# Performance work log

Measured on AMD Instinct MI355X. Metric: run time of the kernel, lower is better.

Reference implementation:

```python
import jax, jax.numpy as jnp
import numpy as np

P = 30000      # nodes (WSI patches)
DIN = 1536     # input feature dim
DOUT = 256     # output dim
HEADS = 2
C = DOUT // HEADS  # per-head channels = 128
E = 320000     # edges (before self-loops)
NEG_SLOPE = 0.2


def setup_inputs() -> dict:
    key = jax.random.key(0)
    ks = jax.random.split(key, 12)
    g = lambda k, shape: jax.random.normal(k, shape, jnp.float32) * 0.02
    return {
        "x": jax.random.normal(ks[0], (P, DIN), jnp.float32),
        "edge_index": jax.random.randint(ks[1], (2, E), 0, P),
        "W1l": g(ks[2], (DIN, DOUT)), "b1l": jnp.zeros((DOUT,), jnp.float32),
        "W1r": g(ks[3], (DIN, DOUT)), "b1r": jnp.zeros((DOUT,), jnp.float32),
        "att1": g(ks[4], (HEADS, C)), "bias1": jnp.zeros((DOUT,), jnp.float32),
        "W2l": g(ks[5], (DOUT, DOUT)), "b2l": jnp.zeros((DOUT,), jnp.float32),
        "W2r": g(ks[6], (DOUT, DOUT)), "b2r": jnp.zeros((DOUT,), jnp.float32),
        "att2": g(ks[7], (HEADS, C)), "bias2": jnp.zeros((DOUT,), jnp.float32),
        "ln1_g": jnp.ones((DOUT,), jnp.float32), "ln1_b": jnp.zeros((DOUT,), jnp.float32),
        "ln2_g": jnp.ones((DOUT,), jnp.float32), "ln2_b": jnp.zeros((DOUT,), jnp.float32),
        "resW": g(ks[8], (DIN, DOUT)), "resb": jnp.zeros((DOUT,), jnp.float32),
    }


def layer_norm(h, g, b, eps=1e-5):
    mu = h.mean(-1, keepdims=True)
    var = ((h - mu) ** 2).mean(-1, keepdims=True)
    return (h - mu) * jax.lax.rsqrt(var + eps) * g + b


def gatv2(x, src, dst, Wl, bl, Wr, br, att, bias):
    # PyG GATv2Conv: lin_l on source j, lin_r on target i,
    # e_ij = att . LeakyReLU(xl[j] + xr[i]); softmax over incoming edges of i;
    # out_i = sum_j alpha_ij * xl[j]  (heads concatenated) + bias.
    n = x.shape[0]
    xl = (x @ Wl + bl).reshape(n, HEADS, C)
    xr = (x @ Wr + br).reshape(n, HEADS, C)
    m = jax.nn.leaky_relu(xl[src] + xr[dst], NEG_SLOPE)      # (Etot, H, C)
    e = jnp.einsum('ehc,hc->eh', m, att)                     # (Etot, H)
    emax = jax.ops.segment_max(e, dst, num_segments=n)       # stable segment softmax
    ex = jnp.exp(e - emax[dst])
    den = jax.ops.segment_sum(ex, dst, num_segments=n)
    alpha = ex / den[dst]                                    # (Etot, H)
    out = jax.ops.segment_sum(xl[src] * alpha[..., None], dst, num_segments=n)
    return out.reshape(n, HEADS * C) + bias


def reference(x, edge_index, W1l, b1l, W1r, b1r, att1, bias1,
              W2l, b2l, W2r, b2r, att2, bias2,
              ln1_g, ln1_b, ln2_g, ln2_b, resW, resb):
    loops = jnp.arange(P)
    src = jnp.concatenate([edge_index[0], loops])  # add self loops
    dst = jnp.concatenate([edge_index[1], loops])

    h1 = gatv2(x, src, dst, W1l, b1l, W1r, b1r, att1, bias1)
    h1 = jax.nn.elu(layer_norm(h1, ln1_g, ln1_b)) + (x @ resW + resb)

    h2 = gatv2(h1, src, dst, W2l, b2l, W2r, b2r, att2, bias2)
    h2 = jax.nn.elu(layer_norm(h2, ln2_g, ln2_b)) + h2 * 0 + h1 + (h2 - h1) * 0 if False else jax.nn.elu(layer_norm(h2, ln2_g, ln2_b)) + h1
    # JK-max combine of the two layer outputs
    return jnp.maximum(h1, h2)
```

## Files before the change

### kernel.cpp

```cpp
#include <hip/hip_runtime.h>
#include <math.h>

#define P_NODES 30000
#define P_PAD   30080
#define DIN_    1536
#define DOUT_   256
#define E_EDGES 320000
#define ET      (E_EDGES + P_NODES)
#define NEG     0.2f
#define BIG_NEG (-1e30f)

typedef float  f32x4  __attribute__((ext_vector_type(4)));
typedef __bf16 bf16x8 __attribute__((ext_vector_type(8)));
typedef __bf16 bf16x4 __attribute__((ext_vector_type(4)));

__device__ __forceinline__ int swz_col(int c, int row) {
    return (c & ~63) | ((((c >> 3) ^ row) & 7) << 3) | (c & 7);
}

__device__ __forceinline__ int xcd_swz(int orig, int nwg) {
    int q = nwg >> 3, r = nwg & 7;
    int xcd = orig & 7, idx = orig >> 3;
    return (xcd < r ? xcd * (q + 1) : r * (q + 1) + (xcd - r) * q) + idx;
}

__global__ __launch_bounds__(256)
void cast_x(const float* __restrict__ x, __bf16* __restrict__ XB)
{
    int idx = blockIdx.x * 256 + threadIdx.x;
    if (idx >= P_PAD * 192) return;
    int row = idx / 192;
    int c = (idx - row * 192) * 8;
    int cs = swz_col(c, row);
    bf16x8 o;
    if (row < P_NODES) {
        f32x4 v0 = *(const f32x4*)(x + (size_t)row * DIN_ + c);
        f32x4 v1 = *(const f32x4*)(x + (size_t)row * DIN_ + c + 4);
        #pragma unroll
        for (int j = 0; j < 4; ++j) { o[j] = (__bf16)v0[j]; o[j + 4] = (__bf16)v1[j]; }
    } else {
        #pragma unroll
        for (int j = 0; j < 8; ++j) o[j] = (__bf16)0.f;
    }
    *(bf16x8*)(XB + (size_t)row * DIN_ + cs) = o;
}

__global__ __launch_bounds__(256)
void prep_w1(const float* __restrict__ W1l, const float* __restrict__ W1r,
             const float* __restrict__ resW, __bf16* __restrict__ WT1)
{
    int idx = blockIdx.x * 256 + threadIdx.x;
    if (idx >= DIN_ * 192) return;
    int k = idx / 192;
    int n0 = (idx - k * 192) * 4;
    const float* src; int col;
    if (n0 < 256)      { src = W1l;  col = n0; }
    else if (n0 < 512) { src = W1r;  col = n0 - 256; }
    else               { src = resW; col = n0 - 512; }
    f32x4 v = *(const f32x4*)(src + (size_t)k * DOUT_ + col);
    #pragma unroll
    for (int j = 0; j < 4; ++j) {
        int n = n0 + j;
        WT1[(size_t)n * DIN_ + swz_col(k, n)] = (__bf16)v[j];
    }
}

__global__ __launch_bounds__(256)
void prep_w2(const float* __restrict__ W2l, const float* __restrict__ W2r,
             __bf16* __restrict__ WT2)
{
    int idx = blockIdx.x * 256 + threadIdx.x;
    if (idx >= 256 * 128) return;
    int k = idx / 128;
    int n0 = (idx - k * 128) * 4;
    const float* src; int col;
    if (n0 < 256) { src = W2l; col = n0; }
    else          { src = W2r; col = n0 - 256; }
    f32x4 v = *(const f32x4*)(src + (size_t)k * DOUT_ + col);
    #pragma unroll
    for (int j = 0; j < 4; ++j) {
        int n = n0 + j;
        WT2[(size_t)n * DOUT_ + swz_col(k, n)] = (__bf16)v[j];
    }
}

__global__ void prep_bias(const float* b1l, const float* b1r, const float* resb,
                          const float* b2l, const float* b2r,
                          float* B1, float* B2)
{
    int t = threadIdx.x;
    if (t < 256)      B1[t] = b1l[t];
    else if (t < 512) B1[t] = b1r[t - 256];
    else if (t < 768) B1[t] = resb[t - 512];
    if (t < 256)      B2[t] = b2l[t];
    else if (t < 512) B2[t] = b2r[t - 256];
}

__global__ void init_deg(int* deg)
{
    int i = blockIdx.x * 256 + threadIdx.x;
    if (i < P_NODES) deg[i] = 1;
}

__global__ void hist_kernel(const int* __restrict__ dst, int* __restrict__ deg)
{
    int e = blockIdx.x * 256 + threadIdx.x;
    if (e < E_EDGES) atomicAdd(&deg[dst[e]], 1);
}

__global__ __launch_bounds__(1024)
void scan_kernel(const int* __restrict__ deg, int* __restrict__ offs, int* __restrict__ pos)
{
    __shared__ int sb[1024];
    const int t = threadIdx.x;
    const int base = t * 30;
    int ldv[30];
    int lsum = 0;
    #pragma unroll
    for (int i = 0; i < 30; ++i) {
        int idx = base + i;
        int v = (idx < P_NODES) ? deg[idx] : 0;
        ldv[i] = v; lsum += v;
    }
    sb[t] = lsum; __syncthreads();
    for (int off = 1; off < 1024; off <<= 1) {
        int v = (t >= off) ? sb[t - off] : 0;
        __syncthreads();
        sb[t] += v;
        __syncthreads();
    }
    int excl = sb[t] - lsum;
    #pragma unroll
    for (int i = 0; i < 30; ++i) {
        int idx = base + i;
        if (idx < P_NODES) { offs[idx] = excl; pos[idx] = excl; excl += ldv[i]; }
    }
    if (t == 0) offs[P_NODES] = ET;
}

__global__ void scatter_kernel(const int* __restrict__ ei, int* __restrict__ pos,
                               int* __restrict__ srcs)
{
    int tgt = blockIdx.x * 256 + threadIdx.x;
    if (tgt < E_EDGES) {
        int s = ei[tgt];
        int d = ei[E_EDGES + tgt];
        int p = atomicAdd(&pos[d], 1);
        srcs[p] = s;
    } else if (tgt < ET) {
        int i = tgt - E_EDGES;
        int p = atomicAdd(&pos[i], 1);
        srcs[p] = i;
    }
}

template<int EPI>
__global__ __launch_bounds__(256)
void gemm_kernel(const __bf16* __restrict__ A, const __bf16* __restrict__ WT,
                 const float* __restrict__ bias,
                 __bf16* __restrict__ Cb, float* __restrict__ Cf,
                 int M, int N, int K, int ntiles)
{
    __shared__ __align__(16) __bf16 As[128 * 64];
    __shared__ __align__(16) __bf16 Bs[128 * 64];

    const int bid = xcd_swz(blockIdx.x, gridDim.x);
    const int mt = bid / ntiles, nt = bid - mt * ntiles;
    const int grow = mt * 128, gcol = nt * 128;
    const int t = threadIdx.x;
    const int lane = t & 63, wave = t >> 6;
    const int wr = wave >> 1, wc = wave & 1;
    const int fr = lane & 15, kg = lane >> 4;
    const int frs = fr & 7;

    const __bf16* agp = A  + (size_t)(grow + (t >> 3)) * K + (t & 7) * 8;
    const __bf16* bgp = WT + (size_t)(gcol + (t >> 3)) * K + (t & 7) * 8;
    const size_t rstep = (size_t)32 * K;
    char* lA = (char*)As + wave * 1024;
    char* lB = (char*)Bs + wave * 1024;

    f32x4 acc[4][4] = {};

    for (int k0 = 0; k0 < K; k0 += 64) {
        __syncthreads();
        #pragma unroll
        for (int i = 0; i < 4; ++i) {
            __builtin_amdgcn_global_load_lds(
                (const __attribute__((address_space(1))) void*)(agp + i * rstep + k0),
                (__attribute__((address_space(3))) void*)(lA + i * 4096), 16, 0, 0);
            __builtin_amdgcn_global_load_lds(
                (const __attribute__((address_space(1))) void*)(bgp + i * rstep + k0),
                (__attribute__((address_space(3))) void*)(lB + i * 4096), 16, 0, 0);
        }
        __syncthreads();

        #pragma unroll
        for (int ks = 0; ks < 2; ++ks) {
            bf16x8 af[4], bv[4];
            #pragma unroll
            for (int mi = 0; mi < 4; ++mi)
                af[mi] = *(const bf16x8*)&As[(wr * 64 + mi * 16 + fr) * 64 + (((ks * 4 + kg) ^ frs)) * 8];
            #pragma unroll
            for (int ni = 0; ni < 4; ++ni)
                bv[ni] = *(const bf16x8*)&Bs[(wc * 64 + ni * 16 + fr) * 64 + (((ks * 4 + kg) ^ frs)) * 8];
            #pragma unroll
            for (int mi = 0; mi < 4; ++mi)
                #pragma unroll
                for (int ni = 0; ni < 4; ++ni)
                    acc[mi][ni] = __builtin_amdgcn_mfma_f32_16x16x32_bf16(af[mi], bv[ni], acc[mi][ni], 0, 0, 0);
        }
    }

    #pragma unroll
    for (int mi = 0; mi < 4; ++mi) {
        #pragma unroll
        for (int ni = 0; ni < 4; ++ni) {
            int col = gcol + wc * 64 + ni * 16 + fr;
            float bvv = bias[col];
            #pragma unroll
            for (int j = 0; j < 4; ++j) {
                int row = grow + wr * 64 + mi * 16 + kg * 4 + j;
                if (row < M) {
                    float v = acc[mi][ni][j] + bvv;
                    if (EPI == 0) {
                        if (col < 512) Cb[(size_t)row * 512 + col] = (__bf16)v;
                        else           Cf[(size_t)row * 256 + col - 512] = v;
                    } else {
                        Cb[(size_t)row * 512 + col] = (__bf16)v;
                    }
                }
            }
        }
    }
}

template<int LAYER>
__global__ __launch_bounds__(256)
void gat_fused(const __bf16* __restrict__ XLXR,
               const int* __restrict__ offs, const int* __restrict__ srcs,
               const float* __restrict__ att, const float* __restrict__ bias,
               const float* __restrict__ lng, const float* __restrict__ lnb,
               const float* __restrict__ AUX,
               float* __restrict__ OutF, __bf16* __restrict__ OutB)
{
    const int node = blockIdx.x * 4 + (threadIdx.x >> 6);
    const int lane = threadIdx.x & 63;
    const int grp = lane >> 4, l = lane & 15;
    const int ch0 = l * 8, ch1 = 128 + l * 8;

    bf16x8 xr0b = *(const bf16x8*)(XLXR + (size_t)node * 512 + 256 + ch0);
    bf16x8 xr1b = *(const bf16x8*)(XLXR + (size_t)node * 512 + 256 + ch1);
    float xr0[8], xr1[8], at0[8], at1[8];
    #pragma unroll
    for (int j = 0; j < 8; ++j) { xr0[j] = (float)xr0b[j]; xr1[j] = (float)xr1b[j]; }
    *(f32x4*)(at0)     = *(const f32x4*)(att + ch0);
    *(f32x4*)(at0 + 4) = *(const f32x4*)(att + ch0 + 4);
    *(f32x4*)(at1)     = *(const f32x4*)(att + ch1);
    *(f32x4*)(at1 + 4) = *(const f32x4*)(att + ch1 + 4);

    float m0 = BIG_NEG, m1 = BIG_NEG, den0 = 0.f, den1 = 0.f;
    float acc0[8] = {}, acc1[8] = {};

    const int e0 = offs[node], e1 = offs[node + 1];
    for (int eb = e0; eb < e1; eb += 4) {
        int e = eb + grp;
        bool valid = e < e1;
        int ee = valid ? e : e1 - 1;
        int s = srcs[ee];
        const __bf16* xp = XLXR + (size_t)s * 512;
        bf16x8 a0 = *(const bf16x8*)(xp + ch0);
        bf16x8 a1 = *(const bf16x8*)(xp + ch1);
        float xl0[8], xl1[8];
        float p0 = 0.f, p1 = 0.f;
        #pragma unroll
        for (int j = 0; j < 8; ++j) {
            xl0[j] = (float)a0[j];
            float tt = xl0[j] + xr0[j];
            float lr = tt > 0.f ? tt : NEG * tt;
            p0 = fmaf(at0[j], lr, p0);
            xl1[j] = (float)a1[j];
            float t1 = xl1[j] + xr1[j];
            float l1 = t1 > 0.f ? t1 : NEG * t1;
            p1 = fmaf(at1[j], l1, p1);
        }
        #pragma unroll
        for (int w = 1; w < 16; w <<= 1) {
            p0 += __shfl_xor(p0, w);
            p1 += __shfl_xor(p1, w);
        }
        if (!valid) { p0 = BIG_NEG; p1 = BIG_NEG; }
        float nm0 = fmaxf(m0, p0), nm1 = fmaxf(m1, p1);
        float sc0 = __expf(m0 - nm0), wv0 = __expf(p0 - nm0);
        float sc1 = __expf(m1 - nm1), wv1 = __expf(p1 - nm1);
        den0 = den0 * sc0 + wv0;
        den1 = den1 * sc1 + wv1;
        #pragma unroll
        for (int j = 0; j < 8; ++j) {
            acc0[j] = acc0[j] * sc0 + wv0 * xl0[j];
            acc1[j] = acc1[j] * sc1 + wv1 * xl1[j];
        }
        m0 = nm0; m1 = nm1;
    }

    #pragma unroll
    for (int w = 16; w <= 32; w <<= 1) {
        float mb0 = __shfl_xor(m0, w), db0 = __shfl_xor(den0, w);
        float mb1 = __shfl_xor(m1, w), db1 = __shfl_xor(den1, w);
        float M0 = fmaxf(m0, mb0), M1 = fmaxf(m1, mb1);
        float sa0 = __expf(m0 - M0), sb0 = __expf(mb0 - M0);
        float sa1 = __expf(m1 - M1), sb1 = __expf(mb1 - M1);
        den0 = den0 * sa0 + db0 * sb0;
        den1 = den1 * sa1 + db1 * sb1;
        #pragma unroll
        for (int j = 0; j < 8; ++j) {
            float ab0 = __shfl_xor(acc0[j], w);
            float ab1 = __shfl_xor(acc1[j], w);
            acc0[j] = acc0[j] * sa0 + ab0 * sb0;
            acc1[j] = acc1[j] * sa1 + ab1 * sb1;
        }
        m0 = M0; m1 = M1;
    }

    float inv0 = 1.f / den0, inv1 = 1.f / den1;
    float o0[8], o1[8];
    #pragma unroll
    for (int j = 0; j < 8; ++j) {
        o0[j] = acc0[j] * inv0 + bias[ch0 + j];
        o1[j] = acc1[j] * inv1 + bias[ch1 + j];
    }

    float s = 0.f;
    #pragma unroll
    for (int j = 0; j < 8; ++j) s += o0[j] + o1[j];
    #pragma unroll
    for (int w = 1; w < 16; w <<= 1) s += __shfl_xor(s, w);
    float mu = s * (1.f / 256.f);
    float sq = 0.f;
    #pragma unroll
    for (int j = 0; j < 8; ++j) {
        o0[j] -= mu; o1[j] -= mu;
        sq += o0[j] * o0[j] + o1[j] * o1[j];
    }
    #pragma unroll
    for (int w = 1; w < 16; w <<= 1) sq += __shfl_xor(sq, w);
    float rs = rsqrtf(sq * (1.f / 256.f) + 1e-5f);

    float g0[8], g1[8], bb0[8], bb1[8], x0[8], x1[8];
    *(f32x4*)(g0)      = *(const f32x4*)(lng + ch0);
    *(f32x4*)(g0 + 4)  = *(const f32x4*)(lng + ch0 + 4);
    *(f32x4*)(g1)      = *(const f32x4*)(lng + ch1);
    *(f32x4*)(g1 + 4)  = *(const f32x4*)(lng + ch1 + 4);
    *(f32x4*)(bb0)     = *(const f32x4*)(lnb + ch0);
    *(f32x4*)(bb0 + 4) = *(const f32x4*)(lnb + ch0 + 4);
    *(f32x4*)(bb1)     = *(const f32x4*)(lnb + ch1);
    *(f32x4*)(bb1 + 4) = *(const f32x4*)(lnb + ch1 + 4);
    *(f32x4*)(x0)      = *(const f32x4*)(AUX + (size_t)node * 256 + ch0);
    *(f32x4*)(x0 + 4)  = *(const f32x4*)(AUX + (size_t)node * 256 + ch0 + 4);
    *(f32x4*)(x1)      = *(const f32x4*)(AUX + (size_t)node * 256 + ch1);
    *(f32x4*)(x1 + 4)  = *(const f32x4*)(AUX + (size_t)node * 256 + ch1 + 4);

    float r0[8], r1[8];
    #pragma unroll
    for (int j = 0; j < 8; ++j) {
        float y0 = o0[j] * rs * g0[j] + bb0[j];
        float y1 = o1[j] * rs * g1[j] + bb1[j];
        float e0v = y0 > 0.f ? y0 : __expf(y0) - 1.f;
        float e1v = y1 > 0.f ? y1 : __expf(y1) - 1.f;
        if (LAYER == 1) {
            r0[j] = e0v + x0[j];
            r1[j] = e1v + x1[j];
        } else {
            float h20 = e0v + x0[j];
            float h21 = e1v + x1[j];
            r0[j] = fmaxf(x0[j], h20);
            r1[j] = fmaxf(x1[j], h21);
        }
    }

    if (grp == 0) {
        float* op = OutF + (size_t)node * 256;
        *(f32x4*)(op + ch0)     = *(f32x4*)(r0);
        *(f32x4*)(op + ch0 + 4) = *(f32x4*)(r0 + 4);
        *(f32x4*)(op + ch1)     = *(f32x4*)(r1);
        *(f32x4*)(op + ch1 + 4) = *(f32x4*)(r1 + 4);
        if (LAYER == 1) {
            bf16x8 hb0, hb1;
            #pragma unroll
            for (int j = 0; j < 8; ++j) { hb0[j] = (__bf16)r0[j]; hb1[j] = (__bf16)r1[j]; }
            *(bf16x8*)(OutB + (size_t)node * 256 + swz_col(ch0, node)) = hb0;
            *(bf16x8*)(OutB + (size_t)node * 256 + swz_col(ch1, node)) = hb1;
        }
    }
}

__global__ void pad_h1b(__bf16* __restrict__ H1B)
{
    int i = blockIdx.x * 256 + threadIdx.x;
    if (i >= (P_PAD - P_NODES) * 32) return;
    int row = P_NODES + (i >> 5);
    int c = (i & 31) * 8;
    bf16x8 z;
    #pragma unroll
    for (int j = 0; j < 8; ++j) z[j] = (__bf16)0.f;
    *(bf16x8*)(H1B + (size_t)row * 256 + c) = z;
}

extern "C" void kernel_launch(void* const* d_in, const int* in_sizes, int n_in,
                              void* d_out, int out_size, void* d_ws, size_t ws_size,
                              hipStream_t stream)
{
    const float* x     = (const float*)d_in[0];
    const int*   ei    = (const int*)d_in[1];
    const float* W1l   = (const float*)d_in[2];
    const float* b1l   = (const float*)d_in[3];
    const float* W1r   = (const float*)d_in[4];
    const float* b1r   = (const float*)d_in[5];
    const float* att1  = (const float*)d_in[6];
    const float* bias1 = (const float*)d_in[7];
    const float* W2l   = (const float*)d_in[8];
    const float* b2l   = (const float*)d_in[9];
    const float* W2r   = (const float*)d_in[10];
    const float* b2r   = (const float*)d_in[11];
    const float* att2  = (const float*)d_in[12];
    const float* bias2 = (const float*)d_in[13];
    const float* ln1g  = (const float*)d_in[14];
    const float* ln1b  = (const float*)d_in[15];
    const float* ln2g  = (const float*)d_in[16];
    const float* ln2b  = (const float*)d_in[17];
    const float* resW  = (const float*)d_in[18];
    const float* resb  = (const float*)d_in[19];
    float* out = (float*)d_out;

    char* w = (char*)d_ws;
    auto alloc = [&](size_t bytes) {
        char* r = w;
        w += (bytes + 255) & ~(size_t)255;
        return r;
    };
    __bf16* XB    = (__bf16*)alloc((size_t)P_PAD * DIN_ * 2);
    __bf16* XLR1  = (__bf16*)alloc((size_t)P_NODES * 512 * 2);
    float*  RES   = (float*)alloc((size_t)P_NODES * 256 * 4);
    float*  H1    = (float*)alloc((size_t)P_NODES * 256 * 4);
    __bf16* WT1   = (__bf16*)alloc((size_t)768 * DIN_ * 2);
    __bf16* WT2   = (__bf16*)alloc((size_t)512 * DOUT_ * 2);
    float*  BIAS1 = (float*)alloc(768 * 4);
    float*  BIAS2 = (float*)alloc(512 * 4);
    int*    deg   = (int*)alloc((size_t)P_NODES * 4);
    int*    offs  = (int*)alloc((size_t)(P_NODES + 1) * 4);
    int*    pos   = (int*)alloc((size_t)(P_NODES + 1) * 4);
    int*    srcs  = (int*)alloc((size_t)ET * 4);

    __bf16* XLR2 = (__bf16*)XB;
    __bf16* H1B  = (__bf16*)((char*)XB + (size_t)32 * 1024 * 1024);

    cast_x<<<(P_PAD * 192 + 255) / 256, 256, 0, stream>>>(x, XB);
    prep_w1<<<(DIN_ * 192 + 255) / 256, 256, 0, stream>>>(W1l, W1r, resW, WT1);
    prep_w2<<<(256 * 128 + 255) / 256, 256, 0, stream>>>(W2l, W2r, WT2);
    prep_bias<<<1, 1024, 0, stream>>>(b1l, b1r, resb, b2l, b2r, BIAS1, BIAS2);
    init_deg<<<(P_NODES + 255) / 256, 256, 0, stream>>>(deg);
    hist_kernel<<<(E_EDGES + 255) / 256, 256, 0, stream>>>(ei + E_EDGES, deg);
    scan_kernel<<<1, 1024, 0, stream>>>(deg, offs, pos);
    scatter_kernel<<<(ET + 255) / 256, 256, 0, stream>>>(ei, pos, srcs);

    const int mtiles = P_PAD / 128;

    gemm_kernel<0><<<mtiles * 6, 256, 0, stream>>>(XB, WT1, BIAS1, XLR1, RES, P_NODES, 768, DIN_, 6);
    gat_fused<1><<<P_NODES / 4, 256, 0, stream>>>(XLR1, offs, srcs, att1, bias1,
                                                  ln1g, ln1b, RES, H1, H1B);
    pad_h1b<<<((P_PAD - P_NODES) * 32 + 255) / 256, 256, 0, stream>>>(H1B);

    gemm_kernel<1><<<mtiles * 4, 256, 0, stream>>>(H1B, WT2, BIAS2, XLR2, nullptr, P_NODES, 512, DOUT_, 4);
    gat_fused<2><<<P_NODES / 4, 256, 0, stream>>>(XLR2, offs, srcs, att2, bias2,
                                                  ln2g, ln2b, H1, out, nullptr);
}
```

Measured before the change: 653.6 us.

## Fuse fp32-to-bf16 cast of x into first GEMM A-tile load; memset degree init

Removes the separate cast_x kernel that converted x to a swizzled bf16 buffer, and instead has the first GEMM read fp32 rows directly, convert them in registers and store them swizzled into LDS. This drops a full write and re-read of a roughly 92 MB intermediate. The cost is that A tiles now go through registers instead of the async global_load_lds path, and each A row is re-read in fp32 (twice the bytes) by all six N-tiles. The init_deg kernel is also replaced by a memset, with the self-loop +1 folded into the scan.

```diff
diff --git a/kernel.cpp b/kernel.cpp
--- a/kernel.cpp
+++ b/kernel.cpp
@@ -22,27 +22,6 @@
     int q = nwg >> 3, r = nwg & 7;
     int xcd = orig & 7, idx = orig >> 3;
     return (xcd < r ? xcd * (q + 1) : r * (q + 1) + (xcd - r) * q) + idx;
-}
-
-__global__ __launch_bounds__(256)
-void cast_x(const float* __restrict__ x, __bf16* __restrict__ XB)
-{
-    int idx = blockIdx.x * 256 + threadIdx.x;
-    if (idx >= P_PAD * 192) return;
-    int row = idx / 192;
-    int c = (idx - row * 192) * 8;
-    int cs = swz_col(c, row);
-    bf16x8 o;
-    if (row < P_NODES) {
-        f32x4 v0 = *(const f32x4*)(x + (size_t)row * DIN_ + c);
-        f32x4 v1 = *(const f32x4*)(x + (size_t)row * DIN_ + c + 4);
-        #pragma unroll
-        for (int j = 0; j < 4; ++j) { o[j] = (__bf16)v0[j]; o[j + 4] = (__bf16)v1[j]; }
-    } else {
-        #pragma unroll
-        for (int j = 0; j < 8; ++j) o[j] = (__bf16)0.f;
-    }
-    *(bf16x8*)(XB + (size_t)row * DIN_ + cs) = o;
 }
 
 __global__ __launch_bounds__(256)
@@ -96,12 +75,6 @@
     else if (t < 512) B2[t] = b2r[t - 256];
 }
 
-__global__ void init_deg(int* deg)
-{
-    int i = blockIdx.x * 256 + threadIdx.x;
-    if (i < P_NODES) deg[i] = 1;
-}
-
 __global__ void hist_kernel(const int* __restrict__ dst, int* __restrict__ deg)
 {
     int e = blockIdx.x * 256 + threadIdx.x;
@@ -119,7 +92,7 @@
     #pragma unroll
     for (int i = 0; i < 30; ++i) {
         int idx = base + i;
-        int v = (idx < P_NODES) ? deg[idx] : 0;
+        int v = (idx < P_NODES) ? (deg[idx] + 1) : 0;
         ldv[i] = v; lsum += v;
     }
     sb[t] = lsum; __syncthreads();
@@ -154,9 +127,9 @@
     }
 }
 
-template<int EPI>
+template<int EPI, bool AF32>
 __global__ __launch_bounds__(256)
-void gemm_kernel(const __bf16* __restrict__ A, const __bf16* __restrict__ WT,
+void gemm_kernel(const void* __restrict__ Av, const __bf16* __restrict__ WT,
                  const float* __restrict__ bias,
                  __bf16* __restrict__ Cb, float* __restrict__ Cf,
                  int M, int N, int K, int ntiles)
@@ -173,24 +146,58 @@
     const int fr = lane & 15, kg = lane >> 4;
     const int frs = fr & 7;
 
-    const __bf16* agp = A  + (size_t)(grow + (t >> 3)) * K + (t & 7) * 8;
     const __bf16* bgp = WT + (size_t)(gcol + (t >> 3)) * K + (t & 7) * 8;
     const size_t rstep = (size_t)32 * K;
+    char* lB = (char*)Bs + wave * 1024;
+
+    const int ra = t >> 1, ha = t & 1;
+    const float* axp = nullptr;
+    const __bf16* agp = nullptr;
     char* lA = (char*)As + wave * 1024;
-    char* lB = (char*)Bs + wave * 1024;
+    if constexpr (AF32) {
+        int arow = grow + ra; if (arow > M - 1) arow = M - 1;
+        axp = (const float*)Av + (size_t)arow * K + ha * 32;
+    } else {
+        agp = (const __bf16*)Av + (size_t)(grow + (t >> 3)) * K + (t & 7) * 8;
+    }
 
     f32x4 acc[4][4] = {};
 
     for (int k0 = 0; k0 < K; k0 += 64) {
         __syncthreads();
-        #pragma unroll
-        for (int i = 0; i < 4; ++i) {
-            __builtin_amdgcn_global_load_lds(
-                (const __attribute__((address_space(1))) void*)(agp + i * rstep + k0),
-                (__attribute__((address_space(3))) void*)(lA + i * 4096), 16, 0, 0);
-            __builtin_amdgcn_global_load_lds(
-                (const __attribute__((address_space(1))) void*)(bgp + i * rstep + k0),
-                (__attribute__((address_space(3))) void*)(lB + i * 4096), 16, 0, 0);
+        if constexpr (AF32) {
+            f32x4 v[8];
+            #pragma unroll
+            for (int gi = 0; gi < 4; ++gi) {
+                v[2 * gi]     = *(const f32x4*)(axp + k0 + gi * 8);
+                v[2 * gi + 1] = *(const f32x4*)(axp + k0 + gi * 8 + 4);
+            }
+            #pragma unroll
+            for (int i = 0; i < 4; ++i)
+                __builtin_amdgcn_global_load_lds(
+                    (const __attribute__((address_space(1))) void*)(bgp + i * rstep + k0),
+                    (__attribute__((address_space(3))) void*)(lB + i * 4096), 16, 0, 0);
+            #pragma unroll
+            for (int gi = 0; gi < 4; ++gi) {
+                bf16x8 o;
+                #pragma unroll
+                for (int j = 0; j < 4; ++j) {
+                    o[j]     = (__bf16)v[2 * gi][j];
+                    o[j + 4] = (__bf16)v[2 * gi + 1][j];
+                }
+                int gpos = (ha * 4 + gi) ^ (ra & 7);
+                *(bf16x8*)&As[ra * 64 + gpos * 8] = o;
+            }
+        } else {
+            #pragma unroll
+            for (int i = 0; i < 4; ++i) {
+                __builtin_amdgcn_global_load_lds(
+                    (const __attribute__((address_space(1))) void*)(agp + i * rstep + k0),
+                    (__attribute__((address_space(3))) void*)(lA + i * 4096), 16, 0, 0);
+                __builtin_amdgcn_global_load_lds(
+                    (const __attribute__((address_space(1))) void*)(bgp + i * rstep + k0),
+                    (__attribute__((address_space(3))) void*)(lB + i * 4096), 16, 0, 0);
+            }
         }
         __syncthreads();
 
@@ -437,8 +444,9 @@
         w += (bytes + 255) & ~(size_t)255;
         return r;
     };
-    __bf16* XB    = (__bf16*)alloc((size_t)P_PAD * DIN_ * 2);
     __bf16* XLR1  = (__bf16*)alloc((size_t)P_NODES * 512 * 2);
+    __bf16* XLR2  = (__bf16*)alloc((size_t)P_NODES * 512 * 2);
+    __bf16* H1B   = (__bf16*)alloc((size_t)P_PAD * 256 * 2);
     float*  RES   = (float*)alloc((size_t)P_NODES * 256 * 4);
     float*  H1    = (float*)alloc((size_t)P_NODES * 256 * 4);
     __bf16* WT1   = (__bf16*)alloc((size_t)768 * DIN_ * 2);
@@ -450,26 +458,22 @@
     int*    pos   = (int*)alloc((size_t)(P_NODES + 1) * 4);
     int*    srcs  = (int*)alloc((size_t)ET * 4);
 
-    __bf16* XLR2 = (__bf16*)XB;
-    __bf16* H1B  = (__bf16*)((char*)XB + (size_t)32 * 1024 * 1024);
-
-    cast_x<<<(P_PAD * 192 + 255) / 256, 256, 0, stream>>>(x, XB);
     prep_w1<<<(DIN_ * 192 + 255) / 256, 256, 0, stream>>>(W1l, W1r, resW, WT1);
     prep_w2<<<(256 * 128 + 255) / 256, 256, 0, stream>>>(W2l, W2r, WT2);
     prep_bias<<<1, 1024, 0, stream>>>(b1l, b1r, resb, b2l, b2r, BIAS1, BIAS2);
-    init_deg<<<(P_NODES + 255) / 256, 256, 0, stream>>>(deg);
+    hipMemsetAsync(deg, 0, (size_t)P_NODES * 4, stream);
     hist_kernel<<<(E_EDGES + 255) / 256, 256, 0, stream>>>(ei + E_EDGES, deg);
     scan_kernel<<<1, 1024, 0, stream>>>(deg, offs, pos);
     scatter_kernel<<<(ET + 255) / 256, 256, 0, stream>>>(ei, pos, srcs);
 
     const int mtiles = P_PAD / 128;
 
-    gemm_kernel<0><<<mtiles * 6, 256, 0, stream>>>(XB, WT1, BIAS1, XLR1, RES, P_NODES, 768, DIN_, 6);
+    gemm_kernel<0, true><<<mtiles * 6, 256, 0, stream>>>(x, WT1, BIAS1, XLR1, RES, P_NODES, 768, DIN_, 6);
     gat_fused<1><<<P_NODES / 4, 256, 0, stream>>>(XLR1, offs, srcs, att1, bias1,
                                                   ln1g, ln1b, RES, H1, H1B);
     pad_h1b<<<((P_PAD - P_NODES) * 32 + 255) / 256, 256, 0, stream>>>(H1B);
 
-    gemm_kernel<1><<<mtiles * 4, 256, 0, stream>>>(H1B, WT2, BIAS2, XLR2, nullptr, P_NODES, 512, DOUT_, 4);
+    gemm_kernel<1, false><<<mtiles * 4, 256, 0, stream>>>(H1B, WT2, BIAS2, XLR2, nullptr, P_NODES, 512, DOUT_, 4);
     gat_fused<2><<<P_NODES / 4, 256, 0, stream>>>(XLR2, offs, srcs, att2, bias2,
                                                   ln2g, ln2b, H1, out, nullptr);
 }
```

Measured after the change: 689.3 us. +5.5%, slower.
